# Optimization experiments

Measured on AMD Instinct MI355X. Metric: run time of the kernel, lower is better.

## Reference

```python
import jax, jax.numpy as jnp
import numpy as np

H_DIM = 1152
N_HEADS = 12
HEAD_DIM = H_DIM // N_HEADS  # 96, divisible by 3
SCALE_ROT = 32 // 16  # character_pixel_size // patch_size


def setup_inputs() -> dict:
    key = jax.random.key(0)
    ks = jax.random.split(key, 9)
    std = 1.0 / np.sqrt(H_DIM)
    return {
        "hidden_states": jax.random.normal(ks[0], (8, 1025, H_DIM), dtype=jnp.float32),
        "Wq": jax.random.normal(ks[1], (H_DIM, H_DIM), dtype=jnp.float32) * std,
        "bq": jax.random.normal(ks[2], (H_DIM,), dtype=jnp.float32) * 0.02,
        "Wk": jax.random.normal(ks[3], (H_DIM, H_DIM), dtype=jnp.float32) * std,
        "bk": jax.random.normal(ks[4], (H_DIM,), dtype=jnp.float32) * 0.02,
        "Wv": jax.random.normal(ks[5], (H_DIM, H_DIM), dtype=jnp.float32) * std,
        "bv": jax.random.normal(ks[6], (H_DIM,), dtype=jnp.float32) * 0.02,
        "Wo": jax.random.normal(ks[7], (H_DIM, H_DIM), dtype=jnp.float32) * std,
        "bo": jax.random.normal(ks[8], (H_DIM,), dtype=jnp.float32) * 0.02,
        "rows": 32,
        "cols": 32,
    }


def _rotary_tables(seq_len, rows, cols, dtype):
    # (seq_len, n_triplets) trig tables based on 2-D patch grid position
    inv_freq = 1.0 / (10000.0 ** (jnp.arange(0, HEAD_DIM, 3, dtype=dtype) / (HEAD_DIM * SCALE_ROT)))
    ids = jnp.arange(seq_len)
    cls_offset = 1 if seq_len != rows * cols else 0
    grid_ids = jnp.clip(ids - cls_offset, 0)
    row_ids = (grid_ids // cols).astype(dtype)
    col_ids = (grid_ids % cols).astype(dtype)
    theta = row_ids[:, None] * inv_freq
    psi = col_ids[:, None] * inv_freq
    return jnp.cos(theta), jnp.sin(theta), jnp.cos(psi), jnp.sin(psi)


def _apply_rotary_3d(x, ct, st, cp, sp):
    # x: (b, s, h, d) -> view as (b, s, h, t, 3)
    b, s, h, d = x.shape
    x = x.reshape(b, s, h, d // 3, 3)
    ct = ct[None, :, None, :]
    st = st[None, :, None, :]
    cp = cp[None, :, None, :]
    sp = sp[None, :, None, :]
    x0, x1, x2 = x[..., 0], x[..., 1], x[..., 2]
    r0 = cp * x0 + sp * st * x1 + sp * ct * x2
    r1 = ct * x1 - st * x2
    r2 = -sp * x0 + cp * st * x1 + cp * ct * x2
    return jnp.stack((r0, r1, r2), axis=-1).reshape(b, s, h, d)


def reference(hidden_states, Wq, bq, Wk, bk, Wv, bv, Wo, bo, rows, cols):
    b, s, _ = hidden_states.shape
    dtype = hidden_states.dtype
    scale = HEAD_DIM ** -0.5

    q = (hidden_states @ Wq + bq).reshape(b, s, N_HEADS, HEAD_DIM)
    k = (hidden_states @ Wk + bk).reshape(b, s, N_HEADS, HEAD_DIM)
    v = (hidden_states @ Wv + bv).reshape(b, s, N_HEADS, HEAD_DIM)

    ct, st, cp, sp = _rotary_tables(s, rows, cols, dtype)
    q = _apply_rotary_3d(q, ct, st, cp, sp)
    k = _apply_rotary_3d(k, ct, st, cp, sp)

    # (b, h, s, s) attention scores
    scores = jnp.einsum("bqhd,bkhd->bhqk", q, k) * scale
    probs = jax.nn.softmax(scores.astype(jnp.float32), axis=-1).astype(dtype)
    ctx = jnp.einsum("bhqk,bkhd->bqhd", probs, v).reshape(b, s, H_DIM)
    out = ctx @ Wo + bo
    return out
```

## Files before the change

### kernel.cpp

```cpp
#include <hip/hip_runtime.h>
#include <stdint.h>

#define BATCH 8
#define SEQ   1025
#define HDIM  1152
#define NH    12
#define DH    96
#define MROWS (BATCH*SEQ)
#define N_QKV (3*HDIM)
#define KD    HDIM
#define NTK   36

typedef __attribute__((ext_vector_type(8))) short short8;
typedef __attribute__((ext_vector_type(4))) short short4_;
typedef __attribute__((ext_vector_type(4))) float float4_;
typedef __attribute__((ext_vector_type(16))) float f32x16;

#define AS1 __attribute__((address_space(1)))
#define AS3 __attribute__((address_space(3)))
#define BARM() do { asm volatile("" ::: "memory"); __builtin_amdgcn_s_barrier(); asm volatile("" ::: "memory"); } while (0)

__device__ inline float bf2f(short s) {
  union { unsigned u; float f; } x; x.u = ((unsigned)(unsigned short)s) << 16; return x.f;
}
__device__ inline short f2bf(float f) {
  union { float f; unsigned u; } x; x.f = f;
  unsigned r = (x.u + 0x7fffu + ((x.u >> 16) & 1u)) >> 16;
  return (short)r;
}

__global__ __launch_bounds__(256) void convx(const float* __restrict__ hs, short* __restrict__ X) {
  int i = blockIdx.x * 256 + threadIdx.x;
  float4_ v = ((const float4_*)hs)[i];
  short4_ o;
  o[0] = f2bf(v[0]); o[1] = f2bf(v[1]); o[2] = f2bf(v[2]); o[3] = f2bf(v[3]);
  ((short4_*)X)[i] = o;
}

__global__ __launch_bounds__(256) void convw_t(const float* __restrict__ W0,
                                               const float* __restrict__ W1,
                                               const float* __restrict__ W2,
                                               short* __restrict__ Wt) {
  __shared__ float T[64][65];
  const int z = blockIdx.z;
  const float* W = z == 0 ? W0 : (z == 1 ? W1 : W2);
  const int n0 = blockIdx.x * 64, k0 = blockIdx.y * 64;
  const int tid = threadIdx.x;
  const int r = tid >> 2, cq = (tid & 3) * 16;
#pragma unroll
  for (int u = 0; u < 4; ++u) {
    float4_ v = *(const float4_*)&W[(long)(k0 + r) * HDIM + n0 + cq + u * 4];
    T[r][cq + u * 4 + 0] = v[0]; T[r][cq + u * 4 + 1] = v[1];
    T[r][cq + u * 4 + 2] = v[2]; T[r][cq + u * 4 + 3] = v[3];
  }
  __syncthreads();
  const int n = tid >> 2, kq = (tid & 3) * 16;
  short out[16];
#pragma unroll
  for (int u = 0; u < 16; ++u) out[u] = f2bf(T[kq + u][n]);
  short* dst = Wt + (long)(z * HDIM + n0 + n) * KD + k0 + kq;
  *(short8*)dst = *(short8*)&out[0];
  *(short8*)(dst + 8) = *(short8*)&out[8];
}

template<int OUTF32>
__global__ __launch_bounds__(256, 3) void gemm256(
    const short* __restrict__ A, const short* __restrict__ Bt,
    const float* __restrict__ b0, const float* __restrict__ b1, const float* __restrict__ b2,
    void* __restrict__ Cout, const int N, const int MT) {
  __shared__ alignas(16) short Lds[24576];
  const int tid = threadIdx.x;
  const int l = tid & 63, w = tid >> 6;
  const int lrow = l & 15, lg = l >> 4;
  const int wr = w >> 1, wc = w & 1;

  const int nwg = gridDim.x;
  const int qq = nwg >> 3, r8 = nwg & 7;
  const int xcd = blockIdx.x & 7, loc = blockIdx.x >> 3;
  const int wg = (xcd < r8 ? xcd * (qq + 1) : r8 * (qq + 1) + (xcd - r8) * qq) + loc;
  const int mt = wg % MT, nt = wg / MT;
  const int m0 = mt * 128, n0 = nt * 128;

  const short* asrc[2]; const short* bsrc[2];
#pragma unroll
  for (int i = 0; i < 2; ++i) {
    int p = i * 256 + tid;
    int wl = (p & 7) ^ ((p >> 3) & 7);
    int row = ((p >> 3) << 1) | (wl >> 2);
    int kc = (wl & 3) * 8;
    int ra = m0 + row; if (ra > MROWS - 1) ra = MROWS - 1;
    int rb = n0 + row; if (rb > N - 1) rb = N - 1;
    asrc[i] = A + (long)ra * KD + kc;
    bsrc[i] = Bt + (long)rb * KD + kc;
  }

#define STAGEA(bi, kt_, i) \
  __builtin_amdgcn_global_load_lds((const AS1 void*)(asrc[i] + (kt_) * 32), \
      (AS3 void*)(&Lds[(bi) * 4096 + (i * 256 + tid) * 8]), 16, 0, 0)
#define STAGEB(bi, kt_, i) \
  __builtin_amdgcn_global_load_lds((const AS1 void*)(bsrc[i] + (kt_) * 32), \
      (AS3 void*)(&Lds[12288 + (bi) * 4096 + (i * 256 + tid) * 8]), 16, 0, 0)
#define LDA(dst, abase, mi) { const int row_ = wr * 64 + (mi) * 16 + lrow; \
  dst = *(const short8*)&Lds[(abase) + ((row_ >> 1) << 6) + \
      (((((row_ & 1) << 2) + lg) ^ ((row_ >> 1) & 7)) << 3)]; }
#define LDB(dst, bbase, nj) { const int row_ = wc * 64 + (nj) * 16 + lrow; \
  dst = *(const short8*)&Lds[(bbase) + ((row_ >> 1) << 6) + \
      (((((row_ & 1) << 2) + lg) ^ ((row_ >> 1) & 7)) << 3)]; }
#define MFMA16(a, b, c) __builtin_amdgcn_mfma_f32_16x16x32_bf16(a, b, c, 0, 0, 0)

  float4_ acc[4][4];
#pragma unroll
  for (int mi = 0; mi < 4; ++mi)
#pragma unroll
    for (int nj = 0; nj < 4; ++nj) acc[mi][nj] = (float4_)(0.f);

  STAGEA(0, 0, 0); STAGEA(0, 0, 1); STAGEB(0, 0, 0); STAGEB(0, 0, 1);
  STAGEA(1, 1, 0); STAGEA(1, 1, 1); STAGEB(1, 1, 0); STAGEB(1, 1, 1);
  asm volatile("s_waitcnt vmcnt(4)" ::: "memory");
  BARM();

  for (int kt = 0; kt < NTK; ++kt) {
    const int cur = kt % 3, st = (kt + 2) % 3;
    const bool dost = (kt + 2) < NTK;
    const int abase = cur * 4096, bbase = 12288 + cur * 4096;
    if (dost) {
      STAGEA(st, kt + 2, 0); STAGEA(st, kt + 2, 1);
      STAGEB(st, kt + 2, 0); STAGEB(st, kt + 2, 1);
    }
    short8 a0, a1, a2, a3, bb0, bb1, bb2, bb3;
    LDB(bb0, bbase, 0); LDB(bb1, bbase, 1); LDB(bb2, bbase, 2); LDB(bb3, bbase, 3);
    LDA(a0, abase, 0); LDA(a1, abase, 1); LDA(a2, abase, 2); LDA(a3, abase, 3);
    acc[0][0] = MFMA16(a0, bb0, acc[0][0]);
    acc[0][1] = MFMA16(a0, bb1, acc[0][1]);
    acc[0][2] = MFMA16(a0, bb2, acc[0][2]);
    acc[0][3] = MFMA16(a0, bb3, acc[0][3]);
    acc[1][0] = MFMA16(a1, bb0, acc[1][0]);
    acc[1][1] = MFMA16(a1, bb1, acc[1][1]);
    acc[1][2] = MFMA16(a1, bb2, acc[1][2]);
    acc[1][3] = MFMA16(a1, bb3, acc[1][3]);
    acc[2][0] = MFMA16(a2, bb0, acc[2][0]);
    acc[2][1] = MFMA16(a2, bb1, acc[2][1]);
    acc[2][2] = MFMA16(a2, bb2, acc[2][2]);
    acc[2][3] = MFMA16(a2, bb3, acc[2][3]);
    acc[3][0] = MFMA16(a3, bb0, acc[3][0]);
    acc[3][1] = MFMA16(a3, bb1, acc[3][1]);
    acc[3][2] = MFMA16(a3, bb2, acc[3][2]);
    acc[3][3] = MFMA16(a3, bb3, acc[3][3]);
    if (dost)                asm volatile("s_waitcnt vmcnt(4)" ::: "memory");
    else if (kt == NTK - 2)  asm volatile("s_waitcnt vmcnt(0)" ::: "memory");
    asm volatile("s_waitcnt lgkmcnt(0)" ::: "memory");
    BARM();
  }

  float bias[4];
#pragma unroll
  for (int nj = 0; nj < 4; ++nj) {
    int cn = n0 + wc * 64 + nj * 16 + lrow;
    float bv_ = 0.f;
    if (cn < N) bv_ = (N == HDIM) ? b0[cn]
                                  : (cn < HDIM ? b0[cn] : (cn < 2 * HDIM ? b1[cn - HDIM] : b2[cn - 2 * HDIM]));
    bias[nj] = bv_;
  }
#pragma unroll
  for (int mi = 0; mi < 4; ++mi)
#pragma unroll
    for (int r = 0; r < 4; ++r) {
      int m = m0 + wr * 64 + mi * 16 + lg * 4 + r;
      if (m >= MROWS) continue;
#pragma unroll
      for (int nj = 0; nj < 4; ++nj) {
        int cn = n0 + wc * 64 + nj * 16 + lrow;
        if (cn >= N) continue;
        float v = acc[mi][nj][r] + bias[nj];
        if (OUTF32) ((float*)Cout)[(long)m * N + cn] = v;
        else        ((short*)Cout)[(long)m * N + cn] = f2bf(v);
      }
    }
#undef STAGEA
#undef STAGEB
#undef LDA
#undef LDB
#undef MFMA16
}

__global__ __launch_bounds__(256) void rotary_q(short* __restrict__ QKV,
                                                const int* __restrict__ rowsp,
                                                const int* __restrict__ colsp) {
  int idx = blockIdx.x * 256 + threadIdx.x;
  if (idx >= MROWS * NH * 4) return;
  const int qt = idx & 3;
  const int hm = idx >> 2;
  const int h = hm % NH, m = hm / NH;
  const int s = m % SEQ;
  const int cols = colsp[0], rws = rowsp[0];
  const int off = (SEQ != rws * cols) ? 1 : 0;
  int gid = s - off; if (gid < 0) gid = 0;
  const float frow = (float)(gid / cols), fcol = (float)(gid % cols);
  union { short sh[24]; short8 v[3]; } u;
  short* p = QKV + (long)m * N_QKV + h * DH + qt * 24;
  u.v[0] = *(short8*)p; u.v[1] = *(short8*)(p + 8); u.v[2] = *(short8*)(p + 16);
#pragma unroll
  for (int t = 0; t < 8; ++t) {
    int j = qt * 8 + t;
    float invf = exp2f((float)(3 * j) * (-13.287712379549449f / 192.0f));
    float st, ct, sp, cp;
    __sincosf(frow * invf, &st, &ct);
    __sincosf(fcol * invf, &sp, &cp);
    float x0 = bf2f(u.sh[3 * t]), x1 = bf2f(u.sh[3 * t + 1]), x2 = bf2f(u.sh[3 * t + 2]);
    u.sh[3 * t]     = f2bf( cp * x0 + sp * st * x1 + sp * ct * x2);
    u.sh[3 * t + 1] = f2bf( ct * x1 - st * x2);
    u.sh[3 * t + 2] = f2bf(-sp * x0 + cp * st * x1 + cp * ct * x2);
  }
  *(short8*)p = u.v[0]; *(short8*)(p + 8) = u.v[1]; *(short8*)(p + 16) = u.v[2];
}

__global__ __launch_bounds__(256) void fragpack(const short* __restrict__ QKV,
                                                short* __restrict__ Kf,
                                                short* __restrict__ Vf,
                                                const int* __restrict__ rowsp,
                                                const int* __restrict__ colsp) {
  __shared__ short L[64 * 96];
  const int t = blockIdx.x, bh = blockIdx.y;
  const int b = bh / NH, h = bh % NH;
  const int tid = threadIdx.x;
#pragma unroll
  for (int i = 0; i < 3; ++i) {
    int cc = i * 256 + tid;
    int kv = cc / 384;
    int rm = cc % 384;
    int r = rm / 12, m = rm % 12;
    int s = t * 32 + r; if (s > SEQ - 1) s = SEQ - 1;
    const short* src = QKV + (long)(b * SEQ + s) * N_QKV + (kv ? 2 * HDIM : HDIM) + h * DH + m * 8;
    *(short8*)&L[cc * 8] = *(const short8*)src;
  }
  __syncthreads();
  {
    const int cols = colsp[0], rws = rowsp[0];
    const int off = (SEQ != rws * cols) ? 1 : 0;
#pragma unroll
    for (int i = 0; i < 4; ++i) {
      int idx2 = i * 256 + tid;
      int r = idx2 >> 5, j = idx2 & 31;
      int s = t * 32 + r; if (s > SEQ - 1) s = SEQ - 1;
      int gid = s - off; if (gid < 0) gid = 0;
      float invf = exp2f((float)(3 * j) * (-13.287712379549449f / 192.0f));
      float st, ct, sp, cp;
      __sincosf((float)(gid / cols) * invf, &st, &ct);
      __sincosf((float)(gid % cols) * invf, &sp, &cp);
      short* pp = &L[r * 96 + 3 * j];
      float x0 = bf2f(pp[0]), x1 = bf2f(pp[1]), x2 = bf2f(pp[2]);
      pp[0] = f2bf( cp * x0 + sp * st * x1 + sp * ct * x2);
      pp[1] = f2bf( ct * x1 - st * x2);
      pp[2] = f2bf(-sp * x0 + cp * st * x1 + cp * ct * x2);
    }
  }
  __syncthreads();
#pragma unroll
  for (int i = 0; i < 3; ++i) {
    int oc = i * 256 + tid;
    if (oc < 384) {
      int c = oc / 64, ll = oc & 63;
      int qi = ll & 31, hi = ll >> 5;
      short8 v = *(const short8*)&L[qi * 96 + c * 16 + hi * 8];
      *(short8*)(Kf + (((long)(bh * 33 + t) * 6 + c) * 64 + ll) * 8) = v;
    } else {
      int oc2 = oc - 384;
      int d = oc2 / 128, sl = (oc2 / 64) & 1, ll = oc2 & 63;
      int qi = ll & 31, hi = ll >> 5;
      short8 v;
#pragma unroll
      for (int j = 0; j < 8; ++j)
        v[j] = L[32 * 96 + (sl * 16 + hi * 8 + j) * 96 + d * 32 + qi];
      *(short8*)(Vf + ((((long)(bh * 33 + t) * 3 + d) * 2 + sl) * 64 + ll) * 8) = v;
    }
  }
}

__global__ __launch_bounds__(128, 3) void attn_kernel(const short* __restrict__ QKV,
                                                      const short* __restrict__ Kf,
                                                      const short* __restrict__ Vf,
                                                      short* __restrict__ CTX) {
  const int tid = threadIdx.x;
  const int l = tid & 63, w = tid >> 6;
  const int qi = l & 31, hi = l >> 5;
  const int bid = blockIdx.x;
  const int xcd = bid & 7, jj = bid >> 3;
  const int bh = xcd * 12 + jj / 17;
  const int qb = jj % 17;
  const int b = bh / NH, h = bh % NH;
  const int s = qb * 64 + w * 32 + qi;
  const int sq = s > SEQ - 1 ? SEQ - 1 : s;

  const float scale = 0.1020620726159658f;
  const short* Qr = QKV + (long)(b * SEQ + sq) * N_QKV + h * DH;
  short8 qf[6];
#pragma unroll
  for (int c = 0; c < 6; ++c) {
    short8 v = *(const short8*)(Qr + c * 16 + hi * 8);
#pragma unroll
    for (int j = 0; j < 8; ++j) v[j] = f2bf(bf2f(v[j]) * scale);
    qf[c] = v;
  }

  const short* Kb = Kf + (long)bh * 33 * 6 * 64 * 8;
  const short* Vb = Vf + (long)bh * 33 * 6 * 64 * 8;

  f32x16 ctxv[3];
#pragma unroll
  for (int d = 0; d < 3; ++d) ctxv[d] = (f32x16)(0.f);
  float m_ = -1e30f, l_ = 0.f;

  for (int t = 0; t < 33; ++t) {
    f32x16 S = (f32x16)(0.f);
#pragma unroll
    for (int c = 0; c < 6; ++c) {
      short8 kf = *(const short8*)(Kb + (((long)t * 6 + c) * 64 + l) * 8);
      S = __builtin_amdgcn_mfma_f32_32x32x16_bf16(kf, qf[c], S, 0, 0, 0);
    }
    if (t == 32) {
      S[0] = hi ? -1e30f : S[0];
#pragma unroll
      for (int r = 1; r < 16; ++r) S[r] = -1e30f;
    }
    float tm = S[0];
#pragma unroll
    for (int r = 1; r < 16; ++r) tm = fmaxf(tm, S[r]);
    tm = fmaxf(tm, __shfl_xor(tm, 32));
    if (!__all(tm - m_ <= 8.f)) {
      float mn = fmaxf(m_, tm);
      float alpha = __expf(m_ - mn);
      m_ = mn;
      l_ *= alpha;
#pragma unroll
      for (int d = 0; d < 3; ++d)
#pragma unroll
        for (int r = 0; r < 16; ++r) ctxv[d][r] *= alpha;
    }
    float ts = 0.f;
#pragma unroll
    for (int r = 0; r < 16; ++r) { float p = __expf(S[r] - m_); S[r] = p; ts += p; }
    ts += __shfl_xor(ts, 32);
    l_ += ts;

    unsigned pk_[8];
#pragma unroll
    for (int j = 0; j < 8; ++j)
      pk_[j] = (unsigned)(unsigned short)f2bf(S[2 * j]) |
               ((unsigned)(unsigned short)f2bf(S[2 * j + 1]) << 16);
    unsigned s0 = hi ? pk_[0] : pk_[2];
    unsigned s1 = hi ? pk_[1] : pk_[3];
    unsigned s2 = hi ? pk_[4] : pk_[6];
    unsigned s3 = hi ? pk_[5] : pk_[7];
    unsigned r0 = __shfl_xor(s0, 32);
    unsigned r1 = __shfl_xor(s1, 32);
    unsigned r2 = __shfl_xor(s2, 32);
    unsigned r3 = __shfl_xor(s3, 32);
    union PF { unsigned u[4]; short8 s8; } f0, f1;
    f0.u[0] = hi ? r0 : pk_[0];
    f0.u[1] = hi ? r1 : pk_[1];
    f0.u[2] = hi ? pk_[2] : r0;
    f0.u[3] = hi ? pk_[3] : r1;
    f1.u[0] = hi ? r2 : pk_[4];
    f1.u[1] = hi ? r3 : pk_[5];
    f1.u[2] = hi ? pk_[6] : r2;
    f1.u[3] = hi ? pk_[7] : r3;

#pragma unroll
    for (int d = 0; d < 3; ++d) {
      const short* Vr = Vb + (((long)t * 3 + d) * 2 * 64) * 8;
      short8 vf0 = *(const short8*)(Vr + l * 8);
      ctxv[d] = __builtin_amdgcn_mfma_f32_32x32x16_bf16(vf0, f0.s8, ctxv[d], 0, 0, 0);
      short8 vf1 = *(const short8*)(Vr + (64 + l) * 8);
      ctxv[d] = __builtin_amdgcn_mfma_f32_32x32x16_bf16(vf1, f1.s8, ctxv[d], 0, 0, 0);
    }
  }

  float invl = 1.f / l_;
  if (s <= SEQ - 1) {
    short* Cr = CTX + (long)(b * SEQ + s) * HDIM + h * DH;
#pragma unroll
    for (int d = 0; d < 3; ++d)
#pragma unroll
      for (int g = 0; g < 4; ++g) {
        short4_ o;
#pragma unroll
        for (int r = 0; r < 4; ++r) o[r] = f2bf(ctxv[d][4 * g + r] * invl);
        *(short4_*)(Cr + d * 32 + 8 * g + 4 * hi) = o;
      }
  }
}

extern "C" void kernel_launch(void* const* d_in, const int* in_sizes, int n_in,
                              void* d_out, int out_size, void* d_ws, size_t ws_size,
                              hipStream_t stream) {
  const float* hs = (const float*)d_in[0];
  const float* Wq = (const float*)d_in[1];
  const float* bq = (const float*)d_in[2];
  const float* Wk = (const float*)d_in[3];
  const float* bk = (const float*)d_in[4];
  const float* Wv = (const float*)d_in[5];
  const float* bv = (const float*)d_in[6];
  const float* Wo = (const float*)d_in[7];
  const float* bo = (const float*)d_in[8];
  const int* rows = (const int*)d_in[9];
  const int* cols = (const int*)d_in[10];
  float* out = (float*)d_out;

  char* ws = (char*)d_ws;
  short* X   = (short*)(ws);
  short* Wt  = (short*)(ws + 18892800);
  short* Wot = (short*)(ws + 26855424);
  short* QKV = (short*)(ws + 29509632);
  short* Vf  = (short*)(ws + 86188032);
  short* CTX = (short*)(ws + 105652224);
  short* Kf  = (short*)(ws);

  convx<<<9225, 256, 0, stream>>>(hs, X);
  convw_t<<<dim3(18, 18, 3), 256, 0, stream>>>(Wq, Wk, Wv, Wt);
  convw_t<<<dim3(18, 18, 1), 256, 0, stream>>>(Wo, Wo, Wo, Wot);
  gemm256<0><<<1755, 256, 0, stream>>>(X, Wt, bq, bk, bv, QKV, N_QKV, 65);
  rotary_q<<<1538, 256, 0, stream>>>(QKV, rows, cols);
  fragpack<<<dim3(33, 96), 256, 0, stream>>>(QKV, Kf, Vf, rows, cols);
  attn_kernel<<<1632, 128, 0, stream>>>(QKV, Kf, Vf, CTX);
  gemm256<1><<<585, 256, 0, stream>>>(CTX, Wot, bo, bo, bo, out, HDIM, 65);
}
```

Baseline: 287.2 us.

## Enlarge GEMM tiles to 256x256 with 8 waves and split-K double buffering

The bf16 GEMM kernel goes from 128x128 tiles with 4 waves and a 3-stage 32-wide K pipeline to 256x256 tiles with 8 waves, a 64-wide K step split into two halves, double buffering and a new XOR swizzle. Global-to-LDS loads for the next K step are interleaved between MFMA groups, with s_setprio raised around the MFMAs. This aims to raise arithmetic intensity and cut global traffic per FLOP. The cost is 128KB of LDS per block, fewer blocks (462 and 165 on 256 CUs), and more tile padding waste at the edges. The output projection GEMM in particular may underfill the GPU.

```diff
diff --git a/kernel.cpp b/kernel.cpp
--- a/kernel.cpp
+++ b/kernel.cpp
@@ -9,7 +9,7 @@
 #define MROWS (BATCH*SEQ)
 #define N_QKV (3*HDIM)
 #define KD    HDIM
-#define NTK   36
+#define NT2   18
 
 typedef __attribute__((ext_vector_type(8))) short short8;
 typedef __attribute__((ext_vector_type(4))) short short4_;
@@ -64,91 +64,113 @@
 }
 
 template<int OUTF32>
-__global__ __launch_bounds__(256, 3) void gemm256(
+__global__ __launch_bounds__(512, 2) void gemm256(
     const short* __restrict__ A, const short* __restrict__ Bt,
     const float* __restrict__ b0, const float* __restrict__ b1, const float* __restrict__ b2,
     void* __restrict__ Cout, const int N, const int MT) {
-  __shared__ alignas(16) short Lds[24576];
+  __shared__ alignas(16) short Lds[65536];
   const int tid = threadIdx.x;
   const int l = tid & 63, w = tid >> 6;
   const int lrow = l & 15, lg = l >> 4;
-  const int wr = w >> 1, wc = w & 1;
+  const int wr = w >> 2, wc = w & 3;
 
   const int nwg = gridDim.x;
   const int qq = nwg >> 3, r8 = nwg & 7;
   const int xcd = blockIdx.x & 7, loc = blockIdx.x >> 3;
   const int wg = (xcd < r8 ? xcd * (qq + 1) : r8 * (qq + 1) + (xcd - r8) * qq) + loc;
   const int mt = wg % MT, nt = wg / MT;
-  const int m0 = mt * 128, n0 = nt * 128;
+  const int m0 = mt * 256, n0 = nt * 256;
+
+#define KEYR(r) ((((r) & 3)) ^ (((r) >> 2) & 3))
 
   const short* asrc[2]; const short* bsrc[2];
 #pragma unroll
   for (int i = 0; i < 2; ++i) {
-    int p = i * 256 + tid;
-    int wl = (p & 7) ^ ((p >> 3) & 7);
-    int row = ((p >> 3) << 1) | (wl >> 2);
-    int kc = (wl & 3) * 8;
+    int p = i * 512 + tid;
+    int row = p >> 2;
+    int lslot = (p & 3) ^ KEYR(row);
     int ra = m0 + row; if (ra > MROWS - 1) ra = MROWS - 1;
     int rb = n0 + row; if (rb > N - 1) rb = N - 1;
-    asrc[i] = A + (long)ra * KD + kc;
-    bsrc[i] = Bt + (long)rb * KD + kc;
-  }
-
-#define STAGEA(bi, kt_, i) \
-  __builtin_amdgcn_global_load_lds((const AS1 void*)(asrc[i] + (kt_) * 32), \
-      (AS3 void*)(&Lds[(bi) * 4096 + (i * 256 + tid) * 8]), 16, 0, 0)
-#define STAGEB(bi, kt_, i) \
-  __builtin_amdgcn_global_load_lds((const AS1 void*)(bsrc[i] + (kt_) * 32), \
-      (AS3 void*)(&Lds[12288 + (bi) * 4096 + (i * 256 + tid) * 8]), 16, 0, 0)
-#define LDA(dst, abase, mi) { const int row_ = wr * 64 + (mi) * 16 + lrow; \
-  dst = *(const short8*)&Lds[(abase) + ((row_ >> 1) << 6) + \
-      (((((row_ & 1) << 2) + lg) ^ ((row_ >> 1) & 7)) << 3)]; }
-#define LDB(dst, bbase, nj) { const int row_ = wc * 64 + (nj) * 16 + lrow; \
-  dst = *(const short8*)&Lds[(bbase) + ((row_ >> 1) << 6) + \
-      (((((row_ & 1) << 2) + lg) ^ ((row_ >> 1) & 7)) << 3)]; }
+    asrc[i] = A + (long)ra * KD + lslot * 8;
+    bsrc[i] = Bt + (long)rb * KD + lslot * 8;
+  }
+
+#define STAGEA(sb, kh, kt_, i) \
+  __builtin_amdgcn_global_load_lds((const AS1 void*)(asrc[i] + (kt_) * 64 + (kh) * 32), \
+      (AS3 void*)(&Lds[(sb) * 16384 + (kh) * 8192 + (i * 512 + tid) * 8]), 16, 0, 0)
+#define STAGEB(sb, kh, kt_, i) \
+  __builtin_amdgcn_global_load_lds((const AS1 void*)(bsrc[i] + (kt_) * 64 + (kh) * 32), \
+      (AS3 void*)(&Lds[32768 + (sb) * 16384 + (kh) * 8192 + (i * 512 + tid) * 8]), 16, 0, 0)
+#define LDA(dst, base, mi) { const int row_ = wr * 128 + (mi) * 16 + lrow; \
+  dst = *(const short8*)&Lds[(base) + row_ * 32 + ((lg ^ KEYR(row_)) << 3)]; }
+#define LDB(dst, base, nj) { const int row_ = wc * 64 + (nj) * 16 + lrow; \
+  dst = *(const short8*)&Lds[(base) + row_ * 32 + ((lg ^ KEYR(row_)) << 3)]; }
 #define MFMA16(a, b, c) __builtin_amdgcn_mfma_f32_16x16x32_bf16(a, b, c, 0, 0, 0)
-
-  float4_ acc[4][4];
-#pragma unroll
-  for (int mi = 0; mi < 4; ++mi)
+#define MF16(mb, A0, A1, A2, A3) \
+  acc[(mb)+0][0] = MFMA16(A0, bf0, acc[(mb)+0][0]); \
+  acc[(mb)+0][1] = MFMA16(A0, bf1, acc[(mb)+0][1]); \
+  acc[(mb)+0][2] = MFMA16(A0, bf2, acc[(mb)+0][2]); \
+  acc[(mb)+0][3] = MFMA16(A0, bf3, acc[(mb)+0][3]); \
+  acc[(mb)+1][0] = MFMA16(A1, bf0, acc[(mb)+1][0]); \
+  acc[(mb)+1][1] = MFMA16(A1, bf1, acc[(mb)+1][1]); \
+  acc[(mb)+1][2] = MFMA16(A1, bf2, acc[(mb)+1][2]); \
+  acc[(mb)+1][3] = MFMA16(A1, bf3, acc[(mb)+1][3]); \
+  acc[(mb)+2][0] = MFMA16(A2, bf0, acc[(mb)+2][0]); \
+  acc[(mb)+2][1] = MFMA16(A2, bf1, acc[(mb)+2][1]); \
+  acc[(mb)+2][2] = MFMA16(A2, bf2, acc[(mb)+2][2]); \
+  acc[(mb)+2][3] = MFMA16(A2, bf3, acc[(mb)+2][3]); \
+  acc[(mb)+3][0] = MFMA16(A3, bf0, acc[(mb)+3][0]); \
+  acc[(mb)+3][1] = MFMA16(A3, bf1, acc[(mb)+3][1]); \
+  acc[(mb)+3][2] = MFMA16(A3, bf2, acc[(mb)+3][2]); \
+  acc[(mb)+3][3] = MFMA16(A3, bf3, acc[(mb)+3][3]);
+
+  float4_ acc[8][4];
+#pragma unroll
+  for (int mi = 0; mi < 8; ++mi)
 #pragma unroll
     for (int nj = 0; nj < 4; ++nj) acc[mi][nj] = (float4_)(0.f);
 
-  STAGEA(0, 0, 0); STAGEA(0, 0, 1); STAGEB(0, 0, 0); STAGEB(0, 0, 1);
-  STAGEA(1, 1, 0); STAGEA(1, 1, 1); STAGEB(1, 1, 0); STAGEB(1, 1, 1);
+  STAGEA(0, 0, 0, 0); STAGEA(0, 0, 0, 1);
+  STAGEB(0, 0, 0, 0); STAGEB(0, 0, 0, 1);
+  STAGEA(0, 1, 0, 0); STAGEA(0, 1, 0, 1);
+  STAGEB(0, 1, 0, 0); STAGEB(0, 1, 0, 1);
   asm volatile("s_waitcnt vmcnt(4)" ::: "memory");
   BARM();
 
-  for (int kt = 0; kt < NTK; ++kt) {
-    const int cur = kt % 3, st = (kt + 2) % 3;
-    const bool dost = (kt + 2) < NTK;
-    const int abase = cur * 4096, bbase = 12288 + cur * 4096;
-    if (dost) {
-      STAGEA(st, kt + 2, 0); STAGEA(st, kt + 2, 1);
-      STAGEB(st, kt + 2, 0); STAGEB(st, kt + 2, 1);
-    }
-    short8 a0, a1, a2, a3, bb0, bb1, bb2, bb3;
-    LDB(bb0, bbase, 0); LDB(bb1, bbase, 1); LDB(bb2, bbase, 2); LDB(bb3, bbase, 3);
-    LDA(a0, abase, 0); LDA(a1, abase, 1); LDA(a2, abase, 2); LDA(a3, abase, 3);
-    acc[0][0] = MFMA16(a0, bb0, acc[0][0]);
-    acc[0][1] = MFMA16(a0, bb1, acc[0][1]);
-    acc[0][2] = MFMA16(a0, bb2, acc[0][2]);
-    acc[0][3] = MFMA16(a0, bb3, acc[0][3]);
-    acc[1][0] = MFMA16(a1, bb0, acc[1][0]);
-    acc[1][1] = MFMA16(a1, bb1, acc[1][1]);
-    acc[1][2] = MFMA16(a1, bb2, acc[1][2]);
-    acc[1][3] = MFMA16(a1, bb3, acc[1][3]);
-    acc[2][0] = MFMA16(a2, bb0, acc[2][0]);
-    acc[2][1] = MFMA16(a2, bb1, acc[2][1]);
-    acc[2][2] = MFMA16(a2, bb2, acc[2][2]);
-    acc[2][3] = MFMA16(a2, bb3, acc[2][3]);
-    acc[3][0] = MFMA16(a3, bb0, acc[3][0]);
-    acc[3][1] = MFMA16(a3, bb1, acc[3][1]);
-    acc[3][2] = MFMA16(a3, bb2, acc[3][2]);
-    acc[3][3] = MFMA16(a3, bb3, acc[3][3]);
-    if (dost)                asm volatile("s_waitcnt vmcnt(4)" ::: "memory");
-    else if (kt == NTK - 2)  asm volatile("s_waitcnt vmcnt(0)" ::: "memory");
+  for (int kt = 0; kt < NT2; ++kt) {
+    const int cb = kt & 1, sb = (kt + 1) & 1;
+    const bool dost = (kt + 1) < NT2;
+    const int aK0 = cb * 16384, aK1 = aK0 + 8192;
+    const int bK0 = 32768 + cb * 16384, bK1 = bK0 + 8192;
+    short8 af0, af1, af2, af3, bf0, bf1, bf2, bf3;
+
+    if (dost) { STAGEA(sb, 0, kt + 1, 0); STAGEA(sb, 0, kt + 1, 1); }
+    LDB(bf0, bK0, 0); LDB(bf1, bK0, 1); LDB(bf2, bK0, 2); LDB(bf3, bK0, 3);
+    LDA(af0, aK0, 0); LDA(af1, aK0, 1); LDA(af2, aK0, 2); LDA(af3, aK0, 3);
+    __builtin_amdgcn_s_setprio(1);
+    MF16(0, af0, af1, af2, af3);
+    __builtin_amdgcn_s_setprio(0);
+    if (dost) { STAGEB(sb, 0, kt + 1, 0); STAGEB(sb, 0, kt + 1, 1); }
+    LDA(af0, aK0, 4); LDA(af1, aK0, 5); LDA(af2, aK0, 6); LDA(af3, aK0, 7);
+    __builtin_amdgcn_s_setprio(1);
+    MF16(4, af0, af1, af2, af3);
+    __builtin_amdgcn_s_setprio(0);
+    if (dost) asm volatile("s_waitcnt vmcnt(4)" ::: "memory");
+    else      asm volatile("s_waitcnt vmcnt(0)" ::: "memory");
+    BARM();
+    if (dost) { STAGEA(sb, 1, kt + 1, 0); STAGEA(sb, 1, kt + 1, 1); }
+    LDB(bf0, bK1, 0); LDB(bf1, bK1, 1); LDB(bf2, bK1, 2); LDB(bf3, bK1, 3);
+    LDA(af0, aK1, 0); LDA(af1, aK1, 1); LDA(af2, aK1, 2); LDA(af3, aK1, 3);
+    __builtin_amdgcn_s_setprio(1);
+    MF16(0, af0, af1, af2, af3);
+    __builtin_amdgcn_s_setprio(0);
+    if (dost) { STAGEB(sb, 1, kt + 1, 0); STAGEB(sb, 1, kt + 1, 1); }
+    LDA(af0, aK1, 4); LDA(af1, aK1, 5); LDA(af2, aK1, 6); LDA(af3, aK1, 7);
+    __builtin_amdgcn_s_setprio(1);
+    MF16(4, af0, af1, af2, af3);
+    __builtin_amdgcn_s_setprio(0);
     asm volatile("s_waitcnt lgkmcnt(0)" ::: "memory");
+    asm volatile("s_waitcnt vmcnt(4)" ::: "memory");
     BARM();
   }
 
@@ -162,10 +184,10 @@
     bias[nj] = bv_;
   }
 #pragma unroll
-  for (int mi = 0; mi < 4; ++mi)
+  for (int mi = 0; mi < 8; ++mi)
 #pragma unroll
     for (int r = 0; r < 4; ++r) {
-      int m = m0 + wr * 64 + mi * 16 + lg * 4 + r;
+      int m = m0 + wr * 128 + mi * 16 + lg * 4 + r;
       if (m >= MROWS) continue;
 #pragma unroll
       for (int nj = 0; nj < 4; ++nj) {
@@ -181,6 +203,8 @@
 #undef LDA
 #undef LDB
 #undef MFMA16
+#undef MF16
+#undef KEYR
 }
 
 __global__ __launch_bounds__(256) void rotary_q(short* __restrict__ QKV,
@@ -418,9 +442,9 @@
   convx<<<9225, 256, 0, stream>>>(hs, X);
   convw_t<<<dim3(18, 18, 3), 256, 0, stream>>>(Wq, Wk, Wv, Wt);
   convw_t<<<dim3(18, 18, 1), 256, 0, stream>>>(Wo, Wo, Wo, Wot);
-  gemm256<0><<<1755, 256, 0, stream>>>(X, Wt, bq, bk, bv, QKV, N_QKV, 65);
+  gemm256<0><<<462, 512, 0, stream>>>(X, Wt, bq, bk, bv, QKV, N_QKV, 33);
   rotary_q<<<1538, 256, 0, stream>>>(QKV, rows, cols);
   fragpack<<<dim3(33, 96), 256, 0, stream>>>(QKV, Kf, Vf, rows, cols);
   attn_kernel<<<1632, 128, 0, stream>>>(QKV, Kf, Vf, CTX);
-  gemm256<1><<<585, 256, 0, stream>>>(CTX, Wot, bo, bo, bo, out, HDIM, 65);
-}
+  gemm256<1><<<165, 512, 0, stream>>>(CTX, Wot, bo, bo, bo, out, HDIM, 33);
+}
```

Result: faster. 279.2 us (-2.8%).
